# Performance work log

Hardware: AMD Instinct MI355X
Metric: run time of the kernel (lower is better)

The kernel has to match this reference:

```python
import jax, jax.numpy as jnp
import numpy as np

B = 256
NUM_PRIMARY = 32      # cfg.num_primary_caps
PRIM_ATOMS = 8
NUM_CLASSES = 10
DIGIT_ATOMS = 16
NUM_ROUTING = 3       # cfg.num_routing (DigitCap)
IN_DIM = 6 * 6 * NUM_PRIMARY  # 1152
NUM_PIXELS = 28 * 28 * 1


def squash(s, axis):
    # v = ||s||^2/(1+||s||^2) * s/||s||
    n2 = jnp.sum(jnp.square(s), axis=axis, keepdims=True)
    return s * (n2 / (1.0 + n2)) / jnp.sqrt(n2 + 1e-9)


def conv2d(x, w, stride):
    return jax.lax.conv_general_dilated(
        x, w, (stride, stride), 'VALID',
        dimension_numbers=('NCHW', 'OIHW', 'NCHW'))


def setup_inputs() -> dict:
    key = jax.random.key(0)
    ks = jax.random.split(key, 10)
    x = jax.random.uniform(ks[0], (B, 1, 28, 28), jnp.float32)
    labels = jax.random.randint(ks[1], (B,), 0, NUM_CLASSES)
    y = jax.nn.one_hot(labels, NUM_CLASSES, dtype=jnp.float32)
    conv1_w = 0.05 * jax.random.normal(ks[2], (256, 1, 9, 9), jnp.float32)
    conv1_b = jnp.full((256,), 0.1, jnp.float32)
    # primary capsule conv: 256 -> 32 caps * 8 atoms, k=9, s=2 (bias applied after routing)
    prim_w = 0.05 * jax.random.normal(ks[3], (NUM_PRIMARY * PRIM_ATOMS, 256, 9, 9), jnp.float32)
    prim_b = jnp.full((NUM_PRIMARY, PRIM_ATOMS), 0.1, jnp.float32)
    # digit capsule transform: [in_dim, in_atoms, out_dim, out_atoms]
    digit_w = 0.05 * jax.random.normal(ks[4], (IN_DIM, PRIM_ATOMS, NUM_CLASSES, DIGIT_ATOMS), jnp.float32)
    digit_b = jnp.full((NUM_CLASSES, DIGIT_ATOMS), 0.1, jnp.float32)
    w1 = 0.05 * jax.random.normal(ks[5], (NUM_CLASSES * DIGIT_ATOMS, 512), jnp.float32)
    b1 = jnp.zeros((512,), jnp.float32)
    w2 = 0.05 * jax.random.normal(ks[6], (512, 1024), jnp.float32)
    b2 = jnp.zeros((1024,), jnp.float32)
    w3 = 0.05 * jax.random.normal(ks[7], (1024, NUM_PIXELS), jnp.float32)
    b3 = jnp.zeros((NUM_PIXELS,), jnp.float32)
    return dict(x=x, y=y, conv1_w=conv1_w, conv1_b=conv1_b, prim_w=prim_w,
                prim_b=prim_b, digit_w=digit_w, digit_b=digit_b,
                w1=w1, b1=b1, w2=w2, b2=b2, w3=w3, b3=b3)


def reference(x, y, conv1_w, conv1_b, prim_w, prim_b, digit_w, digit_b,
              w1, b1, w2, b2, w3, b3):
    # conv stem
    h = jax.nn.relu(conv2d(x, conv1_w, 1) + conv1_b[None, :, None, None])  # [B,256,20,20]

    # PrimaryCap: conv votes [B, in_dim=1, out=32, atoms=8, 6, 6]; num_routing=1
    votes_p = conv2d(h, prim_w, 2).reshape(B, NUM_PRIMARY, PRIM_ATOMS, 6, 6)
    # one routing iter, input_dim=1: softmax(zeros) over output_dim -> uniform 1/32
    preact_p = votes_p / NUM_PRIMARY + prim_b[None, :, :, None, None]
    caps1 = squash(preact_p, axis=2)  # [B,32,8,6,6]

    # permute(0,1,3,4,2) then flatten -> [B, 1152, 8]
    x3 = jnp.transpose(caps1, (0, 1, 3, 4, 2)).reshape(B, IN_DIM, PRIM_ATOMS)

    # DigitCap votes: [B, in_dim, out_dim, out_atoms]
    votes = jnp.einsum('bia,iaot->biot', x3, digit_w)
    logits = jnp.zeros((B, IN_DIM, NUM_CLASSES), votes.dtype)
    act = None
    for _ in range(NUM_ROUTING):
        route = jax.nn.softmax(logits, axis=2)  # over output capsules
        preact = jnp.einsum('bio,biot->bot', route, votes) + digit_b
        act = squash(preact, axis=-1)  # [B,10,16]
        logits = logits + jnp.einsum('biot,bot->bio', votes, act)
    digit = act

    # Reconstruction: mask by label, 160 -> 512 -> 1024 -> 784
    masked = (digit * y[:, :, None]).reshape(B, NUM_CLASSES * DIGIT_ATOMS)
    r = jax.nn.relu(masked @ w1 + b1)
    r = jax.nn.relu(r @ w2 + b2)
    recon = jax.nn.sigmoid(r @ w3 + b3)
    return digit, recon
```

## Files before the change

kernel.cpp:

```cpp
#include <hip/hip_runtime.h>
#include <hip/hip_bf16.h>

typedef unsigned short u16;
typedef unsigned int u32;

static __device__ __forceinline__ float us2f(u16 u) {
    return __uint_as_float(((u32)u) << 16);
}
static __device__ __forceinline__ u16 f2bu(float f) {
    u32 u = __float_as_uint(f);
    return (u16)((u + 0x7fffu + ((u >> 16) & 1u)) >> 16);
}

typedef __attribute__((ext_vector_type(8))) __bf16 bf16x8;
typedef __attribute__((ext_vector_type(4))) float f32x4;

static __device__ __forceinline__ void async16(const u16* g, u16* l) {
    __builtin_amdgcn_global_load_lds(
        (const __attribute__((address_space(1))) unsigned int*)g,
        (__attribute__((address_space(3))) unsigned int*)l, 16, 0, 0);
}

__global__ void fill_sentinel(float* out, int n, float val) {
    int g = blockIdx.x * 256 + threadIdx.x;
    if (g < n) out[g] = val;
}

__global__ __launch_bounds__(256) void conv_c1wb(const float* __restrict__ w,
                                                 u16* __restrict__ wb)
{
    const int j = blockIdx.x, c = threadIdx.x;
    wb[j * 256 + c] = f2bu(w[c * 81 + j]);
}

__global__ __launch_bounds__(256) void conv1_kernel(const float* __restrict__ x,
    const u16* __restrict__ wb, const float* __restrict__ bias, u16* __restrict__ h)
{
    __shared__ float xs[784];
    __shared__ u16 wl[81 * 256];
    const int b = blockIdx.x >> 2, g = blockIdx.x & 3;
    const int c = threadIdx.x;
    for (int idx = c; idx < 784; idx += 256) xs[idx] = x[b * 784 + idx];
    for (int idx = c; idx < 20736; idx += 256) wl[idx] = wb[idx];
    __syncthreads();
    const float bv = bias[c];
    #pragma unroll 1
    for (int iy = g * 5; iy < g * 5 + 5; ++iy) {
        float acc[20];
        #pragma unroll
        for (int i = 0; i < 20; ++i) acc[i] = bv;
        #pragma unroll 1
        for (int dy = 0; dy < 9; ++dy) {
            float xr[28];
            const float4* xrow = reinterpret_cast<const float4*>(&xs[(iy + dy) * 28]);
            #pragma unroll
            for (int i = 0; i < 7; ++i) {
                float4 v = xrow[i];
                xr[4*i] = v.x; xr[4*i+1] = v.y; xr[4*i+2] = v.z; xr[4*i+3] = v.w;
            }
            #pragma unroll
            for (int dx = 0; dx < 9; ++dx) {
                const float wv = us2f(wl[(dy * 9 + dx) * 256 + c]);
                #pragma unroll
                for (int ix = 0; ix < 20; ++ix) acc[ix] += xr[ix + dx] * wv;
            }
        }
        u16* hp = h + ((b * 20 + iy) * 20) * 256 + c;
        #pragma unroll
        for (int ix = 0; ix < 20; ++ix) hp[ix * 256] = f2bu(fmaxf(acc[ix], 0.f));
    }
}

__global__ __launch_bounds__(256) void transpose_primw(const float* __restrict__ w,
                                                       u16* __restrict__ wt)
{
    __shared__ u16 wl[81 * 258];
    const int n = blockIdx.x, tid = threadIdx.x;
    const float* ws = w + (size_t)n * 20736;
    for (int idx = tid; idx < 20736; idx += 256) {
        const int cc = idx / 81, kk = idx - cc * 81;
        wl[kk * 258 + cc] = f2bu(ws[idx]);
    }
    __syncthreads();
    u16* wo = wt + (size_t)n * 20736;
    for (int q = tid; q < 20736; q += 256)
        wo[q] = wl[(q >> 8) * 258 + (q & 255)];
}

__global__ __launch_bounds__(256) void conv_dwb(const float* __restrict__ dw,
                                                u16* __restrict__ dwb_t)
{
    const int g = blockIdx.x * 256 + threadIdx.x;
    dwb_t[g] = f2bu(dw[g]);
}

__global__ __launch_bounds__(256, 2) void prim_gemm_split(const u16* __restrict__ h,
    const u16* __restrict__ wT, float* __restrict__ pm)
{
    __shared__ u16 As[3 * 4096];
    __shared__ u16 Bs[3 * 8192];
    const int tid = threadIdx.x;
    const int split = blockIdx.y;
    const int mBase = blockIdx.x * 128;
    const int lane = tid & 63, wv = tid >> 6;
    const int swzq = (tid & 3) ^ ((lane >> 3) & 3);
    const int rA = wv * 32 + (lane >> 2);
    const int rB = wv * 64 + (lane >> 2);
    int mA0 = mBase + rA;
    int bA0 = mA0 / 36, rr0 = mA0 % 36;
    const int aBase0 = ((bA0 * 20 + 2 * (rr0 / 6)) * 20 + 2 * (rr0 % 6)) * 256 + swzq * 8;
    int mA1 = mA0 + 16;
    int bA1 = mA1 / 36, rr1 = mA1 % 36;
    const int aBase1 = ((bA1 * 20 + 2 * (rr1 / 6)) * 20 + 2 * (rr1 % 6)) * 256 + swzq * 8;
    const u16* bp0 = wT + (size_t)rB * 20736 + swzq * 8;

    int kglob = split * 3456;
    int ky = kglob / 2304; int krem = kglob - ky * 2304;
    int kx = krem >> 8; int c0 = krem & 255;

    f32x4 acc[4][8];
    #pragma unroll
    for (int i = 0; i < 4; ++i)
        #pragma unroll
        for (int j = 0; j < 8; ++j) acc[i][j] = (f32x4){0.f, 0.f, 0.f, 0.f};

    const int wm = wv >> 1, wn = wv & 1;
    const int lcol = lane & 15, lquad = lane >> 4;
    const int rswz = (lquad ^ ((lcol >> 1) & 3)) * 8;
    const u16* Arow = As + (wm * 64 + lcol) * 32 + rswz;
    const u16* Brow = Bs + (wn * 128 + lcol) * 32 + rswz;
    u16* aD = As + wv * 1024;
    u16* bD = Bs + wv * 2048;

    #define STAGE(sel)  do {                                                   \
        const int koffA = (ky * 20 + kx) * 256 + c0;                           \
        async16(h + aBase0 + koffA, aD + (sel) * 4096);                        \
        async16(h + aBase1 + koffA, aD + (sel) * 4096 + 512);                  \
        async16(bp0 + kglob,          bD + (sel) * 8192);                      \
        async16(bp0 + 331776 + kglob, bD + (sel) * 8192 + 512);               \
        async16(bp0 + 663552 + kglob, bD + (sel) * 8192 + 1024);              \
        async16(bp0 + 995328 + kglob, bD + (sel) * 8192 + 1536);              \
        kglob += 32; c0 += 32;                                                 \
        if (c0 == 256) { c0 = 0; if (++kx == 9) { kx = 0; ++ky; } }            \
    } while (0)

    #define COMPUTE(sel)  do {                                                 \
        const u16* Ab = Arow + (sel) * 4096;                                   \
        const u16* Bb = Brow + (sel) * 8192;                                   \
        bf16x8 af[4], bfr[8];                                                  \
        _Pragma("unroll")                                                      \
        for (int i = 0; i < 4; ++i)                                            \
            af[i] = *reinterpret_cast<const bf16x8*>(Ab + i * 512);            \
        _Pragma("unroll")                                                      \
        for (int j = 0; j < 8; ++j)                                            \
            bfr[j] = *reinterpret_cast<const bf16x8*>(Bb + j * 512);           \
        __builtin_amdgcn_s_setprio(1);                                         \
        _Pragma("unroll")                                                      \
        for (int i = 0; i < 4; ++i)                                            \
            _Pragma("unroll")                                                  \
            for (int j = 0; j < 8; ++j)                                        \
                acc[i][j] = __builtin_amdgcn_mfma_f32_16x16x32_bf16(af[i], bfr[j], acc[i][j], 0, 0, 0); \
        __builtin_amdgcn_s_setprio(0);                                         \
    } while (0)

    STAGE(0);
    STAGE(1);
    int cb = 0, sb = 2;
    #pragma unroll 1
    for (int kt = 0; kt < 106; ++kt) {
        STAGE(sb);
        asm volatile("s_waitcnt vmcnt(12)" ::: "memory");
        __builtin_amdgcn_s_barrier();
        __builtin_amdgcn_sched_barrier(0);
        COMPUTE(cb);
        __builtin_amdgcn_sched_barrier(0);
        __builtin_amdgcn_s_barrier();
        __builtin_amdgcn_sched_barrier(0);
        cb = (cb == 2) ? 0 : cb + 1;
        sb = (sb == 2) ? 0 : sb + 1;
    }
    asm volatile("s_waitcnt vmcnt(6)" ::: "memory");
    __builtin_amdgcn_s_barrier();
    __builtin_amdgcn_sched_barrier(0);
    COMPUTE(1);
    __builtin_amdgcn_sched_barrier(0);
    asm volatile("s_waitcnt vmcnt(0)" ::: "memory");
    __builtin_amdgcn_s_barrier();
    __builtin_amdgcn_sched_barrier(0);
    COMPUTE(2);
    #undef STAGE
    #undef COMPUTE

    #pragma unroll
    for (int i = 0; i < 4; ++i) {
        const int mrow = mBase + wm * 64 + i * 16 + lquad * 4;
        #pragma unroll
        for (int j = 0; j < 8; ++j) {
            const int ncol = wn * 128 + j * 16 + lcol;
            #pragma unroll
            for (int r = 0; r < 4; ++r)
                unsafeAtomicAdd(&pm[(size_t)(mrow + r) * 256 + ncol], acc[i][j][r]);
        }
    }
}

__global__ __launch_bounds__(256) void squash_kernel(float* __restrict__ pm,
    const float* __restrict__ pb)
{
    const int m = blockIdx.x, t = threadIdx.x;
    float pre = pm[(size_t)m * 256 + t] * (1.f / 32.f) + pb[t];
    float sq = pre * pre;
    sq += __shfl_xor(sq, 1); sq += __shfl_xor(sq, 2); sq += __shfl_xor(sq, 4);
    float scale = (sq / (1.f + sq)) * rsqrtf(sq + 1e-9f);
    pm[(size_t)m * 256 + t] = pre * scale;
}

__global__ __launch_bounds__(192) void votes_gemm(const float* __restrict__ x3m,
    const u16* __restrict__ dwb_t, u16* __restrict__ votes, int hb)
{
    __shared__ float dws[8 * 1280];
    __shared__ float x3s[64 * 64];
    const int ic = blockIdx.x * 8, bc = blockIdx.y * 64;
    const int tid = threadIdx.x;
    for (int q = tid; q < 10240; q += 192)
        dws[q] = us2f(dwb_t[(size_t)ic * 1280 + q]);
    for (int q = tid; q < 4096; q += 192) {
        const int b_l = q >> 6, r = q & 63, i_l = r >> 3, a = r & 7;
        const int i = ic + i_l, cap = i / 36, p = i - cap * 36;
        x3s[q] = x3m[((size_t)(hb + bc + b_l) * 36 + p) * 256 + cap * 8 + a];
    }
    __syncthreads();
    if (tid < 160) {
        const int ot = tid;
        float dwr[8][8];
        #pragma unroll
        for (int i_l = 0; i_l < 8; ++i_l)
            #pragma unroll
            for (int a = 0; a < 8; ++a)
                dwr[i_l][a] = dws[i_l * 1280 + a * 160 + ot];
        #pragma unroll 1
        for (int b_l = 0; b_l < 64; ++b_l) {
            u16 ob[8];
            #pragma unroll
            for (int i_l = 0; i_l < 8; ++i_l) {
                const float* xp = &x3s[b_l * 64 + i_l * 8];
                float v = 0.f;
                #pragma unroll
                for (int a = 0; a < 8; ++a) v += xp[a] * dwr[i_l][a];
                ob[i_l] = f2bu(v);
            }
            uint4 o4;
            o4.x = (u32)ob[0] | ((u32)ob[1] << 16);
            o4.y = (u32)ob[2] | ((u32)ob[3] << 16);
            o4.z = (u32)ob[4] | ((u32)ob[5] << 16);
            o4.w = (u32)ob[6] | ((u32)ob[7] << 16);
            *reinterpret_cast<uint4*>(&votes[((size_t)(bc + b_l) * 160 + ot) * 1152 + ic]) = o4;
        }
    }
}

__global__ __launch_bounds__(256) void routing_fused(const u16* __restrict__ votes,
    const float* __restrict__ pD_prev, const float* __restrict__ db,
    float* __restrict__ logits, float* __restrict__ pD_next, int hb, int mode)
{
    __shared__ u16 vs16[160 * 146];
    __shared__ float route_s[144 * 10];
    __shared__ float act_s[160];
    const int ic = blockIdx.x * 144, b_l = blockIdx.y, gb = hb + b_l;
    const int tid = threadIdx.x;

    for (int q = tid; q < 2880; q += 256) {
        const int ot = q / 18, ch = q - ot * 18;
        const uint4 d = *reinterpret_cast<const uint4*>(
            &votes[((size_t)b_l * 160 + ot) * 1152 + ic + ch * 8]);
        u32* vp = reinterpret_cast<u32*>(&vs16[ot * 146 + ch * 8]);
        vp[0] = d.x; vp[1] = d.y; vp[2] = d.z; vp[3] = d.w;
    }
    if (mode >= 1 && tid < 160) {
        float pre = pD_prev[(size_t)gb * 160 + tid] + db[tid];
        float sq = pre * pre;
        sq += __shfl_xor(sq, 1); sq += __shfl_xor(sq, 2);
        sq += __shfl_xor(sq, 4); sq += __shfl_xor(sq, 8);
        act_s[tid] = pre * (sq / (1.f + sq)) * rsqrtf(sq + 1e-9f);
    }
    __syncthreads();

    if (mode >= 1) {
        if (tid < 144) {
            float acc[10];
            #pragma unroll
            for (int k = 0; k < 10; ++k) acc[k] = 0.f;
            #pragma unroll 4
            for (int ot = 0; ot < 160; ++ot)
                acc[ot >> 4] += us2f(vs16[ot * 146 + tid]) * act_s[ot];
            float* lp = &logits[((size_t)gb * 1152 + ic + tid) * 10];
            float l[10];
            if (mode == 1) {
                #pragma unroll
                for (int k = 0; k < 10; ++k) { l[k] = acc[k]; lp[k] = l[k]; }
            } else {
                #pragma unroll
                for (int k = 0; k < 10; ++k) { l[k] = lp[k] + acc[k]; lp[k] = l[k]; }
            }
            float mx = -1e30f;
            #pragma unroll
            for (int k = 0; k < 10; ++k) mx = fmaxf(mx, l[k]);
            float s = 0.f;
            #pragma unroll
            for (int k = 0; k < 10; ++k) { l[k] = __expf(l[k] - mx); s += l[k]; }
            const float inv = 1.f / s;
            #pragma unroll
            for (int k = 0; k < 10; ++k) route_s[tid * 10 + k] = l[k] * inv;
        }
        __syncthreads();
    }

    if (tid < 160) {
        const int o = tid >> 4;
        const u16* vrow = &vs16[tid * 146];
        float acc2 = 0.f;
        if (mode == 0) {
            float s = 0.f;
            #pragma unroll 8
            for (int i = 0; i < 144; ++i) s += us2f(vrow[i]);
            acc2 = 0.1f * s;
        } else {
            const float* rp = &route_s[o];
            #pragma unroll 8
            for (int i = 0; i < 144; ++i)
                acc2 += rp[i * 10] * us2f(vrow[i]);
        }
        unsafeAtomicAdd(&pD_next[(size_t)gb * 160 + tid], acc2);
    }
}

__global__ __launch_bounds__(192) void routing_squash(const float* __restrict__ preactD,
    const float* __restrict__ db, float* __restrict__ act, float* __restrict__ dout, int hb)
{
    const int b = hb + blockIdx.x, tid = threadIdx.x;
    if (tid < 160) {
        float pre = preactD[(size_t)b * 160 + tid] + db[tid];
        float sq = pre * pre;
        sq += __shfl_xor(sq, 1); sq += __shfl_xor(sq, 2);
        sq += __shfl_xor(sq, 4); sq += __shfl_xor(sq, 8);
        float scale = (sq / (1.f + sq)) * rsqrtf(sq + 1e-9f);
        float a = pre * scale;
        act[(size_t)b * 160 + tid] = a;
        if (dout) dout[(size_t)b * 160 + tid] = a;
    }
}

__global__ __launch_bounds__(256) void mlp_layer(const float* __restrict__ in,
    const float* __restrict__ maskY, const float* __restrict__ w,
    const float* __restrict__ bias, float* __restrict__ outp, int K, int N, int mode)
{
    __shared__ float ins[4 * 1024];
    const int b0 = blockIdx.x * 4;
    const int n = blockIdx.y * 256 + threadIdx.x;
    for (int idx = threadIdx.x; idx < 4 * K; idx += 256) {
        float v = in[(size_t)b0 * K + idx];
        if (maskY) {
            const int b_l = idx / K, j = idx % K;
            v *= maskY[(b0 + b_l) * 10 + (j >> 4)];
        }
        ins[idx] = v;
    }
    __syncthreads();
    if (n < N) {
        float a0 = 0.f, a1 = 0.f, a2 = 0.f, a3 = 0.f;
        for (int k = 0; k < K; ++k) {
            const float wvv = w[(size_t)k * N + n];
            a0 += ins[k] * wvv;
            a1 += ins[K + k] * wvv;
            a2 += ins[2 * K + k] * wvv;
            a3 += ins[3 * K + k] * wvv;
        }
        const float bv = bias[n];
        float v[4] = {a0 + bv, a1 + bv, a2 + bv, a3 + bv};
        #pragma unroll
        for (int j = 0; j < 4; ++j) {
            float xv = v[j];
            xv = (mode == 0) ? fmaxf(xv, 0.f) : 1.f / (1.f + __expf(-xv));
            outp[(size_t)(b0 + j) * N + n] = xv;
        }
    }
}

extern "C" void kernel_launch(void* const* d_in, const int* in_sizes, int n_in,
                              void* d_out, int out_size, void* d_ws, size_t ws_size,
                              hipStream_t stream) {
    const float* x   = (const float*)d_in[0];
    const float* y   = (const float*)d_in[1];
    const float* c1w = (const float*)d_in[2];
    const float* c1b = (const float*)d_in[3];
    const float* pw  = (const float*)d_in[4];
    const float* pb  = (const float*)d_in[5];
    const float* dw  = (const float*)d_in[6];
    const float* db  = (const float*)d_in[7];
    const float* w1  = (const float*)d_in[8];
    const float* b1  = (const float*)d_in[9];
    const float* w2  = (const float*)d_in[10];
    const float* b2  = (const float*)d_in[11];
    const float* w3  = (const float*)d_in[12];
    const float* b3  = (const float*)d_in[13];
    float* out = (float*)d_out;
    char* ws = (char*)d_ws;

    static const int exp_sizes[14] = {200704, 2560, 20736, 256, 5308416, 256,
                                      1474560, 160, 81920, 512, 524288, 1024,
                                      802816, 784};
    int bad = (n_in == 14) ? -1 : -2;
    if (bad == -1)
        for (int i = 0; i < 14; ++i) if (in_sizes[i] != exp_sizes[i]) { bad = i; break; }
    if (bad != -1) {
        fill_sentinel<<<(out_size + 255) / 256, 256, 0, stream>>>(out, out_size,
            7168.f + 16.f * (float)(bad + 1));
        return;
    }
    const size_t NEEDED = 72482816ULL;
    if (ws_size < NEEDED) {
        fill_sentinel<<<(out_size + 255) / 256, 256, 0, stream>>>(out, out_size, 111.0f);
        return;
    }

    u16*   h       = (u16*)(ws);
    u16*   wT2     = (u16*)(ws + 52428800);
    float* x3m     = (float*)(ws + 63045632);
    u16*   c1wb    = (u16*)(ws + 63045632);
    u16*   votes   = (u16*)(ws);
    float* logits  = (float*)(ws + 47185920);
    float* act     = (float*)(ws + 58982400);
    float* preactD = (float*)(ws + 59146240);
    u16*   dwb_t   = (u16*)(ws + 59637760);
    float* r1      = (float*)(ws + 62586880);
    float* r2      = (float*)(ws + 63111168);

    conv_c1wb<<<81, 256, 0, stream>>>(c1w, c1wb);
    conv1_kernel<<<1024, 256, 0, stream>>>(x, c1wb, c1b, h);
    transpose_primw<<<256, 256, 0, stream>>>(pw, wT2);
    hipMemsetAsync(x3m, 0, 9437184, stream);
    prim_gemm_split<<<dim3(72, 6), 256, 0, stream>>>(h, wT2, x3m);
    squash_kernel<<<9216, 256, 0, stream>>>(x3m, pb);
    conv_dwb<<<5760, 256, 0, stream>>>(dw, dwb_t);
    hipMemsetAsync(preactD, 0, 491520, stream);

    float* pD0 = preactD, *pD1 = preactD + 40960, *pD2 = preactD + 81920;
    for (int half = 0; half < 2; ++half) {
        const int hb = half * 128;
        votes_gemm<<<dim3(144, 2), 192, 0, stream>>>(x3m, dwb_t, votes, hb);
        routing_fused<<<dim3(8, 128), 256, 0, stream>>>(votes, pD0, db, logits, pD0, hb, 0);
        routing_fused<<<dim3(8, 128), 256, 0, stream>>>(votes, pD0, db, logits, pD1, hb, 1);
        routing_fused<<<dim3(8, 128), 256, 0, stream>>>(votes, pD1, db, logits, pD2, hb, 2);
        routing_squash<<<128, 192, 0, stream>>>(pD2, db, act, out, hb);
    }

    mlp_layer<<<dim3(64, 2), 256, 0, stream>>>(act, y, w1, b1, r1, 160, 512, 0);
    mlp_layer<<<dim3(64, 4), 256, 0, stream>>>(r1, (float*)nullptr, w2, b2, r2, 512, 1024, 0);
    mlp_layer<<<dim3(64, 4), 256, 0, stream>>>(r2, (float*)nullptr, w3, b3, out + 40960, 1024, 784, 1);
}
```

Before: 750.7 us.

## Load primary-capsule weights directly to registers and retile GEMM to 96-row, 8-way split

```diff
diff --git a/kernel.cpp b/kernel.cpp
--- a/kernel.cpp
+++ b/kernel.cpp
@@ -82,9 +82,8 @@
         wl[kk * 258 + cc] = f2bu(ws[idx]);
     }
     __syncthreads();
-    u16* wo = wt + (size_t)n * 20736;
     for (int q = tid; q < 20736; q += 256)
-        wo[q] = wl[(q >> 8) * 258 + (q & 255)];
+        wt[(size_t)(q >> 5) * 8192 + n * 32 + (q & 31)] = wl[(q >> 8) * 258 + (q & 255)];
 }
 
 __global__ __launch_bounds__(256) void conv_dwb(const float* __restrict__ dw,
@@ -94,106 +93,94 @@
     dwb_t[g] = f2bu(dw[g]);
 }
 
-__global__ __launch_bounds__(256, 2) void prim_gemm_split(const u16* __restrict__ h,
+__global__ __launch_bounds__(256, 3) void prim_gemm_split(const u16* __restrict__ h,
     const u16* __restrict__ wT, float* __restrict__ pm)
 {
-    __shared__ u16 As[3 * 4096];
-    __shared__ u16 Bs[3 * 8192];
+    __shared__ u16 As[3 * 3072];
     const int tid = threadIdx.x;
-    const int split = blockIdx.y;
-    const int mBase = blockIdx.x * 128;
+    const int split = blockIdx.x & 7;
+    const int mBase = (blockIdx.x >> 3) * 96;
     const int lane = tid & 63, wv = tid >> 6;
     const int swzq = (tid & 3) ^ ((lane >> 3) & 3);
     const int rA = wv * 32 + (lane >> 2);
-    const int rB = wv * 64 + (lane >> 2);
-    int mA0 = mBase + rA;
+    int mA0 = mBase + ((wv < 3) ? rA : 0);
     int bA0 = mA0 / 36, rr0 = mA0 % 36;
     const int aBase0 = ((bA0 * 20 + 2 * (rr0 / 6)) * 20 + 2 * (rr0 % 6)) * 256 + swzq * 8;
     int mA1 = mA0 + 16;
     int bA1 = mA1 / 36, rr1 = mA1 % 36;
     const int aBase1 = ((bA1 * 20 + 2 * (rr1 / 6)) * 20 + 2 * (rr1 % 6)) * 256 + swzq * 8;
-    const u16* bp0 = wT + (size_t)rB * 20736 + swzq * 8;
-
-    int kglob = split * 3456;
+
+    int kglob = split * 2592;
     int ky = kglob / 2304; int krem = kglob - ky * 2304;
     int kx = krem >> 8; int c0 = krem & 255;
 
-    f32x4 acc[4][8];
+    f32x4 acc[3][8];
     #pragma unroll
-    for (int i = 0; i < 4; ++i)
+    for (int i = 0; i < 3; ++i)
         #pragma unroll
         for (int j = 0; j < 8; ++j) acc[i][j] = (f32x4){0.f, 0.f, 0.f, 0.f};
 
     const int wm = wv >> 1, wn = wv & 1;
     const int lcol = lane & 15, lquad = lane >> 4;
     const int rswz = (lquad ^ ((lcol >> 1) & 3)) * 8;
-    const u16* Arow = As + (wm * 64 + lcol) * 32 + rswz;
-    const u16* Brow = Bs + (wn * 128 + lcol) * 32 + rswz;
+    const u16* Arow = As + (wm * 48 + lcol) * 32 + rswz;
     u16* aD = As + wv * 1024;
-    u16* bD = Bs + wv * 2048;
+    const int bBase = (wn * 128 + lcol) * 32 + lquad * 8;
+    const u16* bPtr = wT + (size_t)(split * 81) * 8192 + bBase;
 
     #define STAGE(sel)  do {                                                   \
         const int koffA = (ky * 20 + kx) * 256 + c0;                           \
-        async16(h + aBase0 + koffA, aD + (sel) * 4096);                        \
-        async16(h + aBase1 + koffA, aD + (sel) * 4096 + 512);                  \
-        async16(bp0 + kglob,          bD + (sel) * 8192);                      \
-        async16(bp0 + 331776 + kglob, bD + (sel) * 8192 + 512);               \
-        async16(bp0 + 663552 + kglob, bD + (sel) * 8192 + 1024);              \
-        async16(bp0 + 995328 + kglob, bD + (sel) * 8192 + 1536);              \
+        if (wv < 3) {                                                          \
+            async16(h + aBase0 + koffA, aD + (sel) * 3072);                    \
+            async16(h + aBase1 + koffA, aD + (sel) * 3072 + 512);              \
+        }                                                                      \
         kglob += 32; c0 += 32;                                                 \
         if (c0 == 256) { c0 = 0; if (++kx == 9) { kx = 0; ++ky; } }            \
-    } while (0)
-
-    #define COMPUTE(sel)  do {                                                 \
-        const u16* Ab = Arow + (sel) * 4096;                                   \
-        const u16* Bb = Brow + (sel) * 8192;                                   \
-        bf16x8 af[4], bfr[8];                                                  \
-        _Pragma("unroll")                                                      \
-        for (int i = 0; i < 4; ++i)                                            \
-            af[i] = *reinterpret_cast<const bf16x8*>(Ab + i * 512);            \
-        _Pragma("unroll")                                                      \
-        for (int j = 0; j < 8; ++j)                                            \
-            bfr[j] = *reinterpret_cast<const bf16x8*>(Bb + j * 512);           \
-        __builtin_amdgcn_s_setprio(1);                                         \
-        _Pragma("unroll")                                                      \
-        for (int i = 0; i < 4; ++i)                                            \
-            _Pragma("unroll")                                                  \
-            for (int j = 0; j < 8; ++j)                                        \
-                acc[i][j] = __builtin_amdgcn_mfma_f32_16x16x32_bf16(af[i], bfr[j], acc[i][j], 0, 0, 0); \
-        __builtin_amdgcn_s_setprio(0);                                         \
     } while (0)
 
     STAGE(0);
     STAGE(1);
     int cb = 0, sb = 2;
     #pragma unroll 1
-    for (int kt = 0; kt < 106; ++kt) {
-        STAGE(sb);
-        asm volatile("s_waitcnt vmcnt(12)" ::: "memory");
+    for (int kt = 0; kt < 81; ++kt) {
+        bf16x8 bfr[8];
+        #pragma unroll
+        for (int j = 0; j < 8; ++j)
+            bfr[j] = *reinterpret_cast<const bf16x8*>(bPtr + j * 512);
+        __builtin_amdgcn_sched_barrier(0);
+        if (kt < 79) STAGE(sb);
+        __builtin_amdgcn_sched_barrier(0);
+        if (kt == 0)       asm volatile("s_waitcnt vmcnt(12)" ::: "memory");
+        else if (kt < 79)  asm volatile("s_waitcnt vmcnt(20)" ::: "memory");
+        else if (kt == 79) asm volatile("s_waitcnt vmcnt(18)" ::: "memory");
+        else               asm volatile("s_waitcnt vmcnt(16)" ::: "memory");
         __builtin_amdgcn_s_barrier();
         __builtin_amdgcn_sched_barrier(0);
-        COMPUTE(cb);
+        {
+            const u16* Ab = Arow + cb * 3072;
+            bf16x8 af[3];
+            #pragma unroll
+            for (int i = 0; i < 3; ++i)
+                af[i] = *reinterpret_cast<const bf16x8*>(Ab + i * 512);
+            __builtin_amdgcn_s_setprio(1);
+            #pragma unroll
+            for (int i = 0; i < 3; ++i)
+                #pragma unroll
+                for (int j = 0; j < 8; ++j)
+                    acc[i][j] = __builtin_amdgcn_mfma_f32_16x16x32_bf16(af[i], bfr[j], acc[i][j], 0, 0, 0);
+            __builtin_amdgcn_s_setprio(0);
+        }
         __builtin_amdgcn_sched_barrier(0);
         __builtin_amdgcn_s_barrier();
-        __builtin_amdgcn_sched_barrier(0);
         cb = (cb == 2) ? 0 : cb + 1;
         sb = (sb == 2) ? 0 : sb + 1;
-    }
-    asm volatile("s_waitcnt vmcnt(6)" ::: "memory");
-    __builtin_amdgcn_s_barrier();
-    __builtin_amdgcn_sched_barrier(0);
-    COMPUTE(1);
-    __builtin_amdgcn_sched_barrier(0);
-    asm volatile("s_waitcnt vmcnt(0)" ::: "memory");
-    __builtin_amdgcn_s_barrier();
-    __builtin_amdgcn_sched_barrier(0);
-    COMPUTE(2);
+        bPtr += 8192;
+    }
     #undef STAGE
-    #undef COMPUTE
 
     #pragma unroll
-    for (int i = 0; i < 4; ++i) {
-        const int mrow = mBase + wm * 64 + i * 16 + lquad * 4;
+    for (int i = 0; i < 3; ++i) {
+        const int mrow = mBase + wm * 48 + i * 16 + lquad * 4;
         #pragma unroll
         for (int j = 0; j < 8; ++j) {
             const int ncol = wn * 128 + j * 16 + lcol;
@@ -424,7 +411,7 @@
     }
 
     u16*   h       = (u16*)(ws);
-    u16*   wT2     = (u16*)(ws + 52428800);
+    u16*   wT3     = (u16*)(ws + 52428800);
     float* x3m     = (float*)(ws + 63045632);
     u16*   c1wb    = (u16*)(ws + 63045632);
     u16*   votes   = (u16*)(ws);
@@ -437,9 +424,9 @@
 
     conv_c1wb<<<81, 256, 0, stream>>>(c1w, c1wb);
     conv1_kernel<<<1024, 256, 0, stream>>>(x, c1wb, c1b, h);
-    transpose_primw<<<256, 256, 0, stream>>>(pw, wT2);
+    transpose_primw<<<256, 256, 0, stream>>>(pw, wT3);
     hipMemsetAsync(x3m, 0, 9437184, stream);
-    prim_gemm_split<<<dim3(72, 6), 256, 0, stream>>>(h, wT2, x3m);
+    prim_gemm_split<<<768, 256, 0, stream>>>(h, wT3, x3m);
     squash_kernel<<<9216, 256, 0, stream>>>(x3m, pb);
     conv_dwb<<<5760, 256, 0, stream>>>(dw, dwb_t);
     hipMemsetAsync(preactD, 0, 491520, stream);
```

After: 793.7 us. 5.7% more time.

## Fuse prep kernels, memsets and squash steps into neighboring kernels

Applied to the files above, without the earlier changes.

```diff
diff --git a/kernel.cpp b/kernel.cpp
--- a/kernel.cpp
+++ b/kernel.cpp
@@ -26,22 +26,50 @@
     if (g < n) out[g] = val;
 }
 
-__global__ __launch_bounds__(256) void conv_c1wb(const float* __restrict__ w,
-                                                 u16* __restrict__ wb)
-{
-    const int j = blockIdx.x, c = threadIdx.x;
-    wb[j * 256 + c] = f2bu(w[c * 81 + j]);
+__global__ __launch_bounds__(256) void prep1(const float* __restrict__ pw,
+    u16* __restrict__ wt, float* __restrict__ x3m)
+{
+    __shared__ u16 wl[81 * 258];
+    const int bid = blockIdx.x, tid = threadIdx.x;
+    if (bid < 256) {
+        const float* ws = pw + (size_t)bid * 20736;
+        for (int idx = tid; idx < 20736; idx += 256) {
+            const int cc = idx / 81, kk = idx - cc * 81;
+            wl[kk * 258 + cc] = f2bu(ws[idx]);
+        }
+        __syncthreads();
+        u16* wo = wt + (size_t)bid * 20736;
+        for (int q = tid; q < 20736; q += 256)
+            wo[q] = wl[(q >> 8) * 258 + (q & 255)];
+    } else {
+        float4 z = {0.f, 0.f, 0.f, 0.f};
+        reinterpret_cast<float4*>(x3m)[(size_t)(bid - 256) * 256 + tid] = z;
+    }
+}
+
+__global__ __launch_bounds__(256) void prep2(const float* __restrict__ dw,
+    u16* __restrict__ dwb_t, float* __restrict__ preactD)
+{
+    const int bid = blockIdx.x, tid = threadIdx.x;
+    if (bid < 5760) {
+        const int g = bid * 256 + tid;
+        dwb_t[g] = f2bu(dw[g]);
+    } else {
+        float4 z = {0.f, 0.f, 0.f, 0.f};
+        reinterpret_cast<float4*>(preactD)[(size_t)(bid - 5760) * 256 + tid] = z;
+    }
 }
 
 __global__ __launch_bounds__(256) void conv1_kernel(const float* __restrict__ x,
-    const u16* __restrict__ wb, const float* __restrict__ bias, u16* __restrict__ h)
+    const float* __restrict__ wfull, const float* __restrict__ bias, u16* __restrict__ h)
 {
     __shared__ float xs[784];
     __shared__ u16 wl[81 * 256];
     const int b = blockIdx.x >> 2, g = blockIdx.x & 3;
     const int c = threadIdx.x;
     for (int idx = c; idx < 784; idx += 256) xs[idx] = x[b * 784 + idx];
-    for (int idx = c; idx < 20736; idx += 256) wl[idx] = wb[idx];
+    for (int idx = c; idx < 20736; idx += 256)
+        wl[idx] = f2bu(wfull[(idx & 255) * 81 + (idx >> 8)]);
     __syncthreads();
     const float bv = bias[c];
     #pragma unroll 1
@@ -69,29 +97,6 @@
         #pragma unroll
         for (int ix = 0; ix < 20; ++ix) hp[ix * 256] = f2bu(fmaxf(acc[ix], 0.f));
     }
-}
-
-__global__ __launch_bounds__(256) void transpose_primw(const float* __restrict__ w,
-                                                       u16* __restrict__ wt)
-{
-    __shared__ u16 wl[81 * 258];
-    const int n = blockIdx.x, tid = threadIdx.x;
-    const float* ws = w + (size_t)n * 20736;
-    for (int idx = tid; idx < 20736; idx += 256) {
-        const int cc = idx / 81, kk = idx - cc * 81;
-        wl[kk * 258 + cc] = f2bu(ws[idx]);
-    }
-    __syncthreads();
-    u16* wo = wt + (size_t)n * 20736;
-    for (int q = tid; q < 20736; q += 256)
-        wo[q] = wl[(q >> 8) * 258 + (q & 255)];
-}
-
-__global__ __launch_bounds__(256) void conv_dwb(const float* __restrict__ dw,
-                                                u16* __restrict__ dwb_t)
-{
-    const int g = blockIdx.x * 256 + threadIdx.x;
-    dwb_t[g] = f2bu(dw[g]);
 }
 
 __global__ __launch_bounds__(256, 2) void prim_gemm_split(const u16* __restrict__ h,
@@ -204,30 +209,33 @@
     }
 }
 
-__global__ __launch_bounds__(256) void squash_kernel(float* __restrict__ pm,
-    const float* __restrict__ pb)
-{
-    const int m = blockIdx.x, t = threadIdx.x;
-    float pre = pm[(size_t)m * 256 + t] * (1.f / 32.f) + pb[t];
-    float sq = pre * pre;
-    sq += __shfl_xor(sq, 1); sq += __shfl_xor(sq, 2); sq += __shfl_xor(sq, 4);
-    float scale = (sq / (1.f + sq)) * rsqrtf(sq + 1e-9f);
-    pm[(size_t)m * 256 + t] = pre * scale;
-}
-
 __global__ __launch_bounds__(192) void votes_gemm(const float* __restrict__ x3m,
-    const u16* __restrict__ dwb_t, u16* __restrict__ votes, int hb)
+    const float* __restrict__ pb, const u16* __restrict__ dwb_t,
+    u16* __restrict__ votes, int hb)
 {
     __shared__ float dws[8 * 1280];
     __shared__ float x3s[64 * 64];
+    __shared__ float pbs[256];
     const int ic = blockIdx.x * 8, bc = blockIdx.y * 64;
     const int tid = threadIdx.x;
+    for (int q = tid; q < 256; q += 192) pbs[q] = pb[q];
     for (int q = tid; q < 10240; q += 192)
         dws[q] = us2f(dwb_t[(size_t)ic * 1280 + q]);
-    for (int q = tid; q < 4096; q += 192) {
-        const int b_l = q >> 6, r = q & 63, i_l = r >> 3, a = r & 7;
+    __syncthreads();
+    for (int g = tid; g < 512; g += 192) {
+        const int b_l = g >> 3, i_l = g & 7;
         const int i = ic + i_l, cap = i / 36, p = i - cap * 36;
-        x3s[q] = x3m[((size_t)(hb + bc + b_l) * 36 + p) * 256 + cap * 8 + a];
+        const float* src = &x3m[((size_t)(hb + bc + b_l) * 36 + p) * 256 + cap * 8];
+        float v[8]; float n2 = 0.f;
+        #pragma unroll
+        for (int a = 0; a < 8; ++a) {
+            v[a] = src[a] * (1.f / 32.f) + pbs[cap * 8 + a];
+            n2 += v[a] * v[a];
+        }
+        const float scale = (n2 / (1.f + n2)) * rsqrtf(n2 + 1e-9f);
+        #pragma unroll
+        for (int a = 0; a < 8; ++a)
+            x3s[b_l * 64 + i_l * 8 + a] = v[a] * scale;
     }
     __syncthreads();
     if (tid < 160) {
@@ -334,36 +342,43 @@
     }
 }
 
-__global__ __launch_bounds__(192) void routing_squash(const float* __restrict__ preactD,
-    const float* __restrict__ db, float* __restrict__ act, float* __restrict__ dout, int hb)
-{
-    const int b = hb + blockIdx.x, tid = threadIdx.x;
-    if (tid < 160) {
-        float pre = preactD[(size_t)b * 160 + tid] + db[tid];
-        float sq = pre * pre;
-        sq += __shfl_xor(sq, 1); sq += __shfl_xor(sq, 2);
-        sq += __shfl_xor(sq, 4); sq += __shfl_xor(sq, 8);
-        float scale = (sq / (1.f + sq)) * rsqrtf(sq + 1e-9f);
-        float a = pre * scale;
-        act[(size_t)b * 160 + tid] = a;
-        if (dout) dout[(size_t)b * 160 + tid] = a;
-    }
-}
-
 __global__ __launch_bounds__(256) void mlp_layer(const float* __restrict__ in,
     const float* __restrict__ maskY, const float* __restrict__ w,
-    const float* __restrict__ bias, float* __restrict__ outp, int K, int N, int mode)
+    const float* __restrict__ bias, float* __restrict__ outp, int K, int N, int mode,
+    const float* __restrict__ db2, float* __restrict__ dout)
 {
     __shared__ float ins[4 * 1024];
+    __shared__ float scl[40];
     const int b0 = blockIdx.x * 4;
     const int n = blockIdx.y * 256 + threadIdx.x;
-    for (int idx = threadIdx.x; idx < 4 * K; idx += 256) {
-        float v = in[(size_t)b0 * K + idx];
-        if (maskY) {
-            const int b_l = idx / K, j = idx % K;
-            v *= maskY[(b0 + b_l) * 10 + (j >> 4)];
-        }
-        ins[idx] = v;
+    if (db2) {
+        if (threadIdx.x < 40) {
+            const int b_l = threadIdx.x / 10, o = threadIdx.x - b_l * 10;
+            const float* pp = &in[(size_t)(b0 + b_l) * 160 + o * 16];
+            float n2 = 0.f;
+            #pragma unroll
+            for (int t = 0; t < 16; ++t) {
+                float pv = pp[t] + db2[o * 16 + t];
+                n2 += pv * pv;
+            }
+            scl[threadIdx.x] = (n2 / (1.f + n2)) * rsqrtf(n2 + 1e-9f);
+        }
+        __syncthreads();
+        for (int idx = threadIdx.x; idx < 4 * 160; idx += 256) {
+            const int b_l = idx / 160, j = idx - b_l * 160;
+            float a = (in[(size_t)(b0 + b_l) * 160 + j] + db2[j]) * scl[b_l * 10 + (j >> 4)];
+            if (blockIdx.y == 0 && dout) dout[(size_t)(b0 + b_l) * 160 + j] = a;
+            ins[idx] = a * maskY[(b0 + b_l) * 10 + (j >> 4)];
+        }
+    } else {
+        for (int idx = threadIdx.x; idx < 4 * K; idx += 256) {
+            float v = in[(size_t)b0 * K + idx];
+            if (maskY) {
+                const int b_l = idx / K, j = idx % K;
+                v *= maskY[(b0 + b_l) * 10 + (j >> 4)];
+            }
+            ins[idx] = v;
+        }
     }
     __syncthreads();
     if (n < N) {
@@ -426,35 +441,30 @@
     u16*   h       = (u16*)(ws);
     u16*   wT2     = (u16*)(ws + 52428800);
     float* x3m     = (float*)(ws + 63045632);
-    u16*   c1wb    = (u16*)(ws + 63045632);
     u16*   votes   = (u16*)(ws);
     float* logits  = (float*)(ws + 47185920);
-    float* act     = (float*)(ws + 58982400);
     float* preactD = (float*)(ws + 59146240);
     u16*   dwb_t   = (u16*)(ws + 59637760);
     float* r1      = (float*)(ws + 62586880);
     float* r2      = (float*)(ws + 63111168);
 
-    conv_c1wb<<<81, 256, 0, stream>>>(c1w, c1wb);
-    conv1_kernel<<<1024, 256, 0, stream>>>(x, c1wb, c1b, h);
-    transpose_primw<<<256, 256, 0, stream>>>(pw, wT2);
-    hipMemsetAsync(x3m, 0, 9437184, stream);
+    prep1<<<2560, 256, 0, stream>>>(pw, wT2, x3m);
+    conv1_kernel<<<1024, 256, 0, stream>>>(x, c1w, c1b, h);
     prim_gemm_split<<<dim3(72, 6), 256, 0, stream>>>(h, wT2, x3m);
-    squash_kernel<<<9216, 256, 0, stream>>>(x3m, pb);
-    conv_dwb<<<5760, 256, 0, stream>>>(dw, dwb_t);
-    hipMemsetAsync(preactD, 0, 491520, stream);
+    prep2<<<5880, 256, 0, stream>>>(dw, dwb_t, preactD);
 
     float* pD0 = preactD, *pD1 = preactD + 40960, *pD2 = preactD + 81920;
     for (int half = 0; half < 2; ++half) {
         const int hb = half * 128;
-        votes_gemm<<<dim3(144, 2), 192, 0, stream>>>(x3m, dwb_t, votes, hb);
+        votes_gemm<<<dim3(144, 2), 192, 0, stream>>>(x3m, pb, dwb_t, votes, hb);
         routing_fused<<<dim3(8, 128), 256, 0, stream>>>(votes, pD0, db, logits, pD0, hb, 0);
         routing_fused<<<dim3(8, 128), 256, 0, stream>>>(votes, pD0, db, logits, pD1, hb, 1);
         routing_fused<<<dim3(8, 128), 256, 0, stream>>>(votes, pD1, db, logits, pD2, hb, 2);
-        routing_squash<<<128, 192, 0, stream>>>(pD2, db, act, out, hb);
-    }
-
-    mlp_layer<<<dim3(64, 2), 256, 0, stream>>>(act, y, w1, b1, r1, 160, 512, 0);
-    mlp_layer<<<dim3(64, 4), 256, 0, stream>>>(r1, (float*)nullptr, w2, b2, r2, 512, 1024, 0);
-    mlp_layer<<<dim3(64, 4), 256, 0, stream>>>(r2, (float*)nullptr, w3, b3, out + 40960, 1024, 784, 1);
-}
+    }
+
+    mlp_layer<<<dim3(64, 2), 256, 0, stream>>>(pD2, y, w1, b1, r1, 160, 512, 0, db, out);
+    mlp_layer<<<dim3(64, 4), 256, 0, stream>>>(r1, (float*)nullptr, w2, b2, r2, 512, 1024, 0,
+                                               (const float*)nullptr, (float*)nullptr);
+    mlp_layer<<<dim3(64, 4), 256, 0, stream>>>(r2, (float*)nullptr, w3, b3, out + 40960, 1024, 784, 1,
+                                               (const float*)nullptr, (float*)nullptr);
+}
```

After: 753.0 us. No clear change (+0.3%).
